# Kernel optimization log

Measured on AMD Instinct MI355X. Metric: run time of the kernel, lower is better.

## Reference

```python
import jax, jax.numpy as jnp
import numpy as np
from jax import lax

V, D, H, L, K = 50257, 1024, 2048, 6, 3
B, S = 4, 2048
EPS = 1.1920929e-07  # torch.finfo(float32).eps (torch RMSNorm default eps=None)


def rmsnorm(x, w):
    return x * lax.rsqrt(jnp.mean(x * x, axis=-1, keepdims=True) + EPS) * w


def depthwise_conv(x, w, b):
    # x: (B,S,D), w: (D,1,K) depthwise kernel, padding='same' as in torch Conv1d
    y = lax.conv_general_dilated(x.transpose(0, 2, 1), w, (1,), 'SAME',
                                 dimension_numbers=('NCH', 'OIH', 'NCH'),
                                 feature_group_count=x.shape[-1])
    return y.transpose(0, 2, 1) + b


def mingru(x, h0, wz, bz, wh, bh, wo, bo):
    # minGRU: z=sigmoid(Wz x), h_tilde=Wh x, h_t=(1-z_t)h_{t-1}+z_t h_tilde_t (parallel scan)
    z = jax.nn.sigmoid(jnp.einsum('bsd,hd->bsh', x, wz) + bz)
    htil = jnp.einsum('bsd,hd->bsh', x, wh) + bh
    a, bc = 1.0 - z, z * htil

    def comb(c1, c2):
        a1, b1 = c1
        a2, b2 = c2
        return a1 * a2, a2 * b1 + b2

    A, Bc = lax.associative_scan(comb, (a, bc), axis=1)
    h = A * h0[:, None, :] + Bc                      # (B,S,H)
    out = jnp.einsum('bsh,dh->bsd', h, wo) + bo      # project back to model dim
    return out, h[:, -1]


def setup_inputs():
    key = jax.random.key(0)
    ks = jax.random.split(key, 16)
    sc = 0.02
    p = {}
    p['x'] = jax.random.randint(ks[0], (B, S), 0, V)
    p['h_prev'] = jax.random.normal(ks[1], (B, L, H), jnp.float32)
    p['emb'] = jax.random.normal(ks[2], (V, D), jnp.float32) * sc
    p['conv_dw_w'] = jax.random.normal(ks[3], (L, D, 1, K), jnp.float32) * sc
    p['conv_dw_b'] = jnp.zeros((L, D), jnp.float32)
    p['conv_pw_w'] = jax.random.normal(ks[4], (L, D, D), jnp.float32) * sc
    p['conv_pw_b'] = jnp.zeros((L, D), jnp.float32)
    p['n1_w'] = jnp.ones((L, D), jnp.float32)
    p['wz'] = jax.random.normal(ks[5], (L, H, D), jnp.float32) * sc
    p['bz'] = jnp.zeros((L, H), jnp.float32)
    p['wh'] = jax.random.normal(ks[6], (L, H, D), jnp.float32) * sc
    p['bh'] = jnp.zeros((L, H), jnp.float32)
    p['wo'] = jax.random.normal(ks[7], (L, D, H), jnp.float32) * sc
    p['bo'] = jnp.zeros((L, D), jnp.float32)
    p['n2_w'] = jnp.ones((L, D), jnp.float32)
    p['f1_w'] = jax.random.normal(ks[8], (L, H, D), jnp.float32) * sc
    p['f1_b'] = jnp.zeros((L, H), jnp.float32)
    p['f2_w'] = jax.random.normal(ks[9], (L, D, H), jnp.float32) * sc
    p['f2_b'] = jnp.zeros((L, D), jnp.float32)
    p['norm_w'] = jnp.ones((D,), jnp.float32)
    p['out_w'] = jax.random.normal(ks[10], (H, D), jnp.float32) * sc
    p['out_b'] = jnp.zeros((H,), jnp.float32)
    return p


def reference(x, h_prev, emb, conv_dw_w, conv_dw_b, conv_pw_w, conv_pw_b, n1_w,
              wz, bz, wh, bh, wo, bo, n2_w, f1_w, f1_b, f2_w, f2_b,
              norm_w, out_w, out_b):
    xe = emb[x]                                      # (B,S,D)
    h_next = []
    for l in range(L):
        c = depthwise_conv(xe, conv_dw_w[l], conv_dw_b[l])
        c = jnp.einsum('bsd,ed->bse', c, conv_pw_w[l]) + conv_pw_b[l]  # 1x1 conv
        xe = c + xe
        g, hl = mingru(rmsnorm(xe, n1_w[l]), h_prev[:, l],
                       wz[l], bz[l], wh[l], bh[l], wo[l], bo[l])
        xe = g + xe
        f = rmsnorm(xe, n2_w[l])
        f = jnp.einsum('bsd,hd->bsh', f, f1_w[l]) + f1_b[l]
        f = jax.nn.gelu(f, approximate=False)
        f = jnp.einsum('bsh,dh->bsd', f, f2_w[l]) + f2_b[l]
        xe = f + xe
        h_next.append(hl)
    out = jnp.einsum('bsd,hd->bsh', rmsnorm(xe, norm_w), out_w) + out_b
    return out, jnp.stack(h_next, axis=1)             # (B,S,H), (B,L,H)
```

## Files before the change

kernel.cpp:

```cpp
#include <hip/hip_runtime.h>

typedef __bf16 bf16x8 __attribute__((ext_vector_type(8)));
typedef float f32x4 __attribute__((ext_vector_type(4)));

#define DEVI __device__ __forceinline__

namespace {
constexpr int cB = 4, cS = 2048, cD = 1024, cH = 2048, cL = 6;
constexpr int cM = cB * cS;
constexpr float cEPS = 1.1920929e-07f;
constexpr int NCH = 16, CHS = cS / NCH;
}

DEVI unsigned short f2bf(float f) {
  union { float f; unsigned u; } c; c.f = f;
  const unsigned u = c.u;
  return (unsigned short)((u + 0x7fffu + ((u >> 16) & 1u)) >> 16);
}
DEVI float bf2f(unsigned short h) {
  union { unsigned u; float f; } c; c.u = ((unsigned)h) << 16;
  return c.f;
}

DEVI void gld16(const void* g, void* l) {
  __builtin_amdgcn_global_load_lds(
      (__attribute__((address_space(1))) void*)g,
      (__attribute__((address_space(3))) void*)l, 16, 0, 0);
}

union F4 { float4 v; float a[4]; };

__global__ __launch_bounds__(256) void embed_k(const int* __restrict__ x,
    const float* __restrict__ emb, float* __restrict__ xe) {
  const int bs = blockIdx.x;
  const int idx = x[bs];
  const int t = threadIdx.x;
  *(float4*)&xe[(size_t)bs * cD + t * 4] =
      *(const float4*)&emb[(size_t)idx * cD + t * 4];
}

__global__ __launch_bounds__(256) void dwconv_k(const float* __restrict__ xe,
    const float* __restrict__ w, const float* __restrict__ bias,
    unsigned short* __restrict__ out) {
  const int bs = blockIdx.x;
  const int s = bs & (cS - 1);
  const int t = threadIdx.x;
  const int d = t * 4;
  const size_t base = (size_t)bs * cD + d;
  F4 x0, xm, xp, vb;
  x0.v = *(const float4*)&xe[base];
  xm.v = make_float4(0.f, 0.f, 0.f, 0.f);
  xp.v = make_float4(0.f, 0.f, 0.f, 0.f);
  if (s > 0) xm.v = *(const float4*)&xe[base - cD];
  if (s < cS - 1) xp.v = *(const float4*)&xe[base + cD];
  vb.v = *(const float4*)&bias[d];
  unsigned short o[4];
#pragma unroll
  for (int j = 0; j < 4; ++j) {
    const float w0 = w[(d + j) * 3 + 0];
    const float w1 = w[(d + j) * 3 + 1];
    const float w2 = w[(d + j) * 3 + 2];
    o[j] = f2bf(xm.a[j] * w0 + x0.a[j] * w1 + xp.a[j] * w2 + vb.a[j]);
  }
  *(ushort4*)&out[base] = make_ushort4(o[0], o[1], o[2], o[3]);
}

__global__ __launch_bounds__(256) void rmsnorm_k(const float* __restrict__ x,
    const float* __restrict__ w, unsigned short* __restrict__ o) {
  const int row = blockIdx.x;
  const int t = threadIdx.x;
  const size_t base = (size_t)row * cD + t * 4;
  F4 v; v.v = *(const float4*)&x[base];
  float ss = v.a[0]*v.a[0] + v.a[1]*v.a[1] + v.a[2]*v.a[2] + v.a[3]*v.a[3];
#pragma unroll
  for (int off = 32; off > 0; off >>= 1) ss += __shfl_down(ss, off, 64);
  __shared__ float red[4];
  if ((t & 63) == 0) red[t >> 6] = ss;
  __syncthreads();
  const float scale = rsqrtf((red[0]+red[1]+red[2]+red[3]) * (1.f/cD) + cEPS);
  F4 wv; wv.v = *(const float4*)&w[t * 4];
  *(ushort4*)&o[base] = make_ushort4(
      f2bf(v.a[0]*scale*wv.a[0]), f2bf(v.a[1]*scale*wv.a[1]),
      f2bf(v.a[2]*scale*wv.a[2]), f2bf(v.a[3]*scale*wv.a[3]));
}

__global__ __launch_bounds__(256) void cvt_k(const float* __restrict__ s,
    unsigned short* __restrict__ d, int n) {
  const int i = (blockIdx.x * 256 + threadIdx.x) * 4;
  if (i >= n) return;
  F4 v; v.v = *(const float4*)&s[i];
  *(ushort4*)&d[i] = make_ushort4(f2bf(v.a[0]), f2bf(v.a[1]),
                                  f2bf(v.a[2]), f2bf(v.a[3]));
}

template<int N, int K, int EPI>
__global__ __launch_bounds__(256) void gemm_bt(
    const unsigned short* __restrict__ A, const unsigned short* __restrict__ W,
    const float* __restrict__ bias, float* __restrict__ Cf,
    unsigned short* __restrict__ Cb) {
  __shared__ unsigned short As[128 * 32];
  __shared__ unsigned short Bs[128 * 32];
  const int t = threadIdx.x;
  const int lane = t & 63;
  const int wave = t >> 6;
  const int m0 = blockIdx.x * 128;
  const int n0 = blockIdx.y * 128;
  const int wm = (wave >> 1) * 64;
  const int wn = (wave & 1) * 64;
  const int fr = lane & 15;
  const int fk = (lane >> 4) * 8;

  const int arow = t >> 2;
  const int acol = (t & 3) * 8;
  const unsigned short* gA = A + (size_t)(m0 + arow) * K + acol;
  const unsigned short* gB = W + (size_t)(n0 + arow) * K + acol;
  unsigned short* lA = As + wave * 512;
  unsigned short* lB = Bs + wave * 512;

  f32x4 acc[4][4] = {};
  for (int k0 = 0; k0 < K; k0 += 32) {
    gld16(gA + k0, lA);
    gld16(gA + k0 + (size_t)64 * K, lA + 2048);
    gld16(gB + k0, lB);
    gld16(gB + k0 + (size_t)64 * K, lB + 2048);
    __syncthreads();
    bf16x8 fa[4], fb[4];
#pragma unroll
    for (int i = 0; i < 4; ++i) {
      fa[i] = *(const bf16x8*)&As[(wm + i * 16 + fr) * 32 + fk];
      fb[i] = *(const bf16x8*)&Bs[(wn + i * 16 + fr) * 32 + fk];
    }
#pragma unroll
    for (int i = 0; i < 4; ++i)
#pragma unroll
      for (int j = 0; j < 4; ++j)
        acc[i][j] = __builtin_amdgcn_mfma_f32_16x16x32_bf16(
            fa[i], fb[j], acc[i][j], 0, 0, 0);
    __syncthreads();
  }

  const int r0 = m0 + wm + ((lane >> 4) << 2);
  const int c0 = n0 + wn + fr;
#pragma unroll
  for (int i = 0; i < 4; ++i)
#pragma unroll
    for (int j = 0; j < 4; ++j) {
      const int col = c0 + j * 16;
      const float bv = bias[col];
#pragma unroll
      for (int r = 0; r < 4; ++r) {
        const size_t idx = (size_t)(r0 + i * 16 + r) * N + col;
        const float v = acc[i][j][r] + bv;
        if constexpr (EPI == 0) {
          Cf[idx] = v;
        } else if constexpr (EPI == 1) {
          Cf[idx] += v;
        } else if constexpr (EPI == 2) {
          Cb[idx] = f2bf(1.f / (1.f + __expf(-v)));
        } else if constexpr (EPI == 3) {
          Cb[idx] = f2bf(v);
        } else {
          Cb[idx] = f2bf(0.5f * v * (1.f + erff(v * 0.70710678118654752f)));
        }
      }
    }
}

__global__ __launch_bounds__(256) void scan1_k(const unsigned short* __restrict__ z,
    const unsigned short* __restrict__ ht, float* __restrict__ Ac,
    float* __restrict__ Bc) {
  const int tid = blockIdx.x * 256 + threadIdx.x;
  const int hp = (tid & (cH / 2 - 1)) * 2;
  const int ck = (tid / (cH / 2)) & (NCH - 1);
  const int b = tid / ((cH / 2) * NCH);
  const size_t base = ((size_t)b * cS + (size_t)ck * CHS) * cH + hp;
  float a0 = 1.f, s0 = 0.f, a1 = 1.f, s1 = 0.f;
#pragma unroll 4
  for (int s = 0; s < CHS; ++s) {
    const unsigned zz = *(const unsigned*)&z[base + (size_t)s * cH];
    const unsigned hh = *(const unsigned*)&ht[base + (size_t)s * cH];
    const float z0 = bf2f((unsigned short)(zz & 0xffff)), z1 = bf2f((unsigned short)(zz >> 16));
    const float t0 = bf2f((unsigned short)(hh & 0xffff)), t1 = bf2f((unsigned short)(hh >> 16));
    const float aa0 = 1.f - z0, aa1 = 1.f - z1;
    s0 = aa0 * s0 + z0 * t0; a0 *= aa0;
    s1 = aa1 * s1 + z1 * t1; a1 *= aa1;
  }
  const size_t so = ((size_t)b * NCH + ck) * cH + hp;
  *(float2*)&Ac[so] = make_float2(a0, a1);
  *(float2*)&Bc[so] = make_float2(s0, s1);
}

__global__ __launch_bounds__(256) void scan2_k(const float* __restrict__ Ac,
    const float* __restrict__ Bc, const float* __restrict__ h_prev,
    float* __restrict__ P, float* __restrict__ hn, int l) {
  const int tid = blockIdx.x * 256 + threadIdx.x;
  const int h = tid & (cH - 1);
  const int b = tid >> 11;
  float run = h_prev[((size_t)b * cL + l) * cH + h];
#pragma unroll
  for (int c = 0; c < NCH; ++c) {
    const size_t so = ((size_t)b * NCH + c) * cH + h;
    P[so] = run;
    run = Ac[so] * run + Bc[so];
  }
  hn[((size_t)b * cL + l) * cH + h] = run;
}

__global__ __launch_bounds__(256) void scan3_k(const unsigned short* __restrict__ z,
    unsigned short* __restrict__ ht, const float* __restrict__ P) {
  const int tid = blockIdx.x * 256 + threadIdx.x;
  const int hp = (tid & (cH / 2 - 1)) * 2;
  const int ck = (tid / (cH / 2)) & (NCH - 1);
  const int b = tid / ((cH / 2) * NCH);
  const size_t base = ((size_t)b * cS + (size_t)ck * CHS) * cH + hp;
  const size_t so = ((size_t)b * NCH + ck) * cH + hp;
  const float2 rr = *(const float2*)&P[so];
  float r0 = rr.x, r1 = rr.y;
#pragma unroll 4
  for (int s = 0; s < CHS; ++s) {
    const unsigned zz = *(const unsigned*)&z[base + (size_t)s * cH];
    const unsigned hh = *(const unsigned*)&ht[base + (size_t)s * cH];
    const float z0 = bf2f((unsigned short)(zz & 0xffff)), z1 = bf2f((unsigned short)(zz >> 16));
    const float t0 = bf2f((unsigned short)(hh & 0xffff)), t1 = bf2f((unsigned short)(hh >> 16));
    r0 = (1.f - z0) * r0 + z0 * t0;
    r1 = (1.f - z1) * r1 + z1 * t1;
    *(unsigned*)&ht[base + (size_t)s * cH] =
        (unsigned)f2bf(r0) | ((unsigned)f2bf(r1) << 16);
  }
}

extern "C" void kernel_launch(void* const* d_in, const int* in_sizes, int n_in,
                              void* d_out, int out_size, void* d_ws, size_t ws_size,
                              hipStream_t stream) {
  (void)in_sizes; (void)n_in; (void)out_size; (void)ws_size;
  const int*   x      = (const int*)d_in[0];
  const float* h_prev = (const float*)d_in[1];
  const float* emb    = (const float*)d_in[2];
  const float* cdw_w  = (const float*)d_in[3];
  const float* cdw_b  = (const float*)d_in[4];
  const float* cpw_w  = (const float*)d_in[5];
  const float* cpw_b  = (const float*)d_in[6];
  const float* n1w    = (const float*)d_in[7];
  const float* wzp    = (const float*)d_in[8];
  const float* bzp    = (const float*)d_in[9];
  const float* whp    = (const float*)d_in[10];
  const float* bhp    = (const float*)d_in[11];
  const float* wop    = (const float*)d_in[12];
  const float* bop    = (const float*)d_in[13];
  const float* n2w    = (const float*)d_in[14];
  const float* f1wp   = (const float*)d_in[15];
  const float* f1bp   = (const float*)d_in[16];
  const float* f2wp   = (const float*)d_in[17];
  const float* f2bp   = (const float*)d_in[18];
  const float* nw     = (const float*)d_in[19];
  const float* owp    = (const float*)d_in[20];
  const float* obp    = (const float*)d_in[21];

  float* out_main = (float*)d_out;
  float* out_hn   = out_main + (size_t)cM * cH;

  char* p = (char*)d_ws;
  auto alloc = [&](size_t bytes) {
    char* r = p; p += (bytes + 255) & ~(size_t)255; return r;
  };
  float*          xe = (float*)alloc((size_t)cM * cD * 4);
  unsigned short* xn = (unsigned short*)alloc((size_t)cM * cD * 2);
  unsigned short* zb = (unsigned short*)alloc((size_t)cM * cH * 2);
  unsigned short* hb = (unsigned short*)alloc((size_t)cM * cH * 2);
  float* Ac = (float*)alloc((size_t)cB * NCH * cH * 4);
  float* Bc = (float*)alloc((size_t)cB * NCH * cH * 4);
  float* Pr = (float*)alloc((size_t)cB * NCH * cH * 4);
  unsigned short* w_pw = (unsigned short*)alloc((size_t)cD * cD * 2);
  unsigned short* w_z  = (unsigned short*)alloc((size_t)cH * cD * 2);
  unsigned short* w_h  = (unsigned short*)alloc((size_t)cH * cD * 2);
  unsigned short* w_o  = (unsigned short*)alloc((size_t)cD * cH * 2);
  unsigned short* w_f1 = (unsigned short*)alloc((size_t)cH * cD * 2);
  unsigned short* w_f2 = (unsigned short*)alloc((size_t)cD * cH * 2);

  auto cvt = [&](const float* src, unsigned short* dst, size_t n) {
    cvt_k<<<dim3((unsigned)(n / 1024)), 256, 0, stream>>>(src, dst, (int)n);
  };

  embed_k<<<cM, 256, 0, stream>>>(x, emb, xe);

  for (int l = 0; l < cL; ++l) {
    cvt(cpw_w + (size_t)l * cD * cD, w_pw, (size_t)cD * cD);
    cvt(wzp  + (size_t)l * cH * cD, w_z,  (size_t)cH * cD);
    cvt(whp  + (size_t)l * cH * cD, w_h,  (size_t)cH * cD);
    cvt(wop  + (size_t)l * cD * cH, w_o,  (size_t)cD * cH);
    cvt(f1wp + (size_t)l * cH * cD, w_f1, (size_t)cH * cD);
    cvt(f2wp + (size_t)l * cD * cH, w_f2, (size_t)cD * cH);

    dwconv_k<<<cM, 256, 0, stream>>>(xe, cdw_w + (size_t)l * cD * 3,
                                     cdw_b + (size_t)l * cD, xn);
    gemm_bt<cD, cD, 1><<<dim3(cM / 128, cD / 128), 256, 0, stream>>>(
        xn, w_pw, cpw_b + (size_t)l * cD, xe, nullptr);

    rmsnorm_k<<<cM, 256, 0, stream>>>(xe, n1w + (size_t)l * cD, xn);
    gemm_bt<cH, cD, 2><<<dim3(cM / 128, cH / 128), 256, 0, stream>>>(
        xn, w_z, bzp + (size_t)l * cH, nullptr, zb);
    gemm_bt<cH, cD, 3><<<dim3(cM / 128, cH / 128), 256, 0, stream>>>(
        xn, w_h, bhp + (size_t)l * cH, nullptr, hb);
    scan1_k<<<cB * NCH * (cH / 2) / 256, 256, 0, stream>>>(zb, hb, Ac, Bc);
    scan2_k<<<cB * cH / 256, 256, 0, stream>>>(Ac, Bc, h_prev, Pr, out_hn, l);
    scan3_k<<<cB * NCH * (cH / 2) / 256, 256, 0, stream>>>(zb, hb, Pr);
    gemm_bt<cD, cH, 1><<<dim3(cM / 128, cD / 128), 256, 0, stream>>>(
        hb, w_o, bop + (size_t)l * cD, xe, nullptr);

    rmsnorm_k<<<cM, 256, 0, stream>>>(xe, n2w + (size_t)l * cD, xn);
    gemm_bt<cH, cD, 4><<<dim3(cM / 128, cH / 128), 256, 0, stream>>>(
        xn, w_f1, f1bp + (size_t)l * cH, nullptr, zb);
    gemm_bt<cD, cH, 1><<<dim3(cM / 128, cD / 128), 256, 0, stream>>>(
        zb, w_f2, f2bp + (size_t)l * cD, xe, nullptr);
  }

  rmsnorm_k<<<cM, 256, 0, stream>>>(xe, nw, xn);
  cvt(owp, w_z, (size_t)cH * cD);
  gemm_bt<cH, cD, 0><<<dim3(cM / 128, cH / 128), 256, 0, stream>>>(
      xn, w_z, obp, out_main, nullptr);
}
```

Measured before the change: 2.397 ms.

## Add 256x256 pipelined 8-wave GEMM, fuse z/h projections, hoist weight conversion

Adds a new 512-thread GEMM kernel with 256x256 tiles, double-buffered LDS, and phased MFMA/load interleaving using barriers and priority hints. It is used for the wide-N GEMMs: the z and h projections are merged into one launch, and the FFN up-projection and output head also use it. Weight conversion to bf16 now runs once for all layers before the loop instead of per layer. The aim is better MFMA utilisation and data reuse, plus fewer launches, at the cost of a larger workspace and high register and LDS pressure.

```diff
diff --git a/kernel.cpp b/kernel.cpp
--- a/kernel.cpp
+++ b/kernel.cpp
@@ -151,19 +151,161 @@
       for (int r = 0; r < 4; ++r) {
         const size_t idx = (size_t)(r0 + i * 16 + r) * N + col;
         const float v = acc[i][j][r] + bv;
-        if constexpr (EPI == 0) {
+        if constexpr (EPI == 1) {
+          Cf[idx] += v;
+        } else {
           Cf[idx] = v;
-        } else if constexpr (EPI == 1) {
-          Cf[idx] += v;
-        } else if constexpr (EPI == 2) {
-          Cb[idx] = f2bf(1.f / (1.f + __expf(-v)));
-        } else if constexpr (EPI == 3) {
-          Cb[idx] = f2bf(v);
-        } else {
-          Cb[idx] = f2bf(0.5f * v * (1.f + erff(v * 0.70710678118654752f)));
         }
       }
     }
+}
+
+#define RDA(BUF, MH)                                                        \
+  _Pragma("unroll") for (int mf = 0; mf < 4; ++mf)                          \
+  _Pragma("unroll") for (int kk = 0; kk < 2; ++kk)                          \
+      a[mf * 2 + kk] = *(const bf16x8*)&lds[(BUF)*16384 + aB + (MH)*4096 +  \
+                                            mf * 1024 + kk * 32];
+
+#define RDB(BUF)                                                            \
+  _Pragma("unroll") for (int q = 0; q < 4; ++q)                             \
+  _Pragma("unroll") for (int kk = 0; kk < 2; ++kk)                          \
+      b[q >> 1][(q & 1) * 2 + kk] =                                         \
+          *(const bf16x8*)&lds[(BUF)*16384 + bB + q * 1024 + kk * 32];
+
+#define MMQ(MH, NH)                                                         \
+  _Pragma("unroll") for (int mf = 0; mf < 4; ++mf)                          \
+  _Pragma("unroll") for (int nf = 0; nf < 2; ++nf)                          \
+  _Pragma("unroll") for (int kk = 0; kk < 2; ++kk)                          \
+      acc[(MH)*4 + mf][(NH)*2 + nf] = __builtin_amdgcn_mfma_f32_16x16x32_bf16( \
+          a[mf * 2 + kk], b[NH][nf * 2 + kk], acc[(MH)*4 + mf][(NH)*2 + nf],  \
+          0, 0, 0);
+
+#define PH_SYNC()                                                           \
+  __builtin_amdgcn_s_barrier();                                             \
+  asm volatile("s_waitcnt lgkmcnt(0)" ::: "memory");                        \
+  __builtin_amdgcn_sched_barrier(0);                                        \
+  __builtin_amdgcn_s_setprio(1)
+
+#define PH_END()                                                            \
+  __builtin_amdgcn_s_setprio(0);                                            \
+  __builtin_amdgcn_s_barrier()
+
+#define TILE_PHASES(TI, BUF, OBUF)                                          \
+  {                                                                         \
+    RDA(BUF, 0); RDB(BUF);                                                  \
+    { const int n1 = (TI) + 1;                                              \
+      stA((n1 < NT) ? n1 : 0, 1, (n1 < NT) ? ldsA(OBUF, 1) : ldsDummy); }   \
+    asm volatile("s_waitcnt lgkmcnt(8)" ::: "memory");                      \
+    PH_SYNC(); MMQ(0, 0); PH_END();                                         \
+    { const int n2 = (TI) + 2;                                              \
+      stB((n2 < NT) ? n2 : 0, 0, (n2 < NT) ? ldsB(BUF, 0) : ldsDummy); }    \
+    PH_SYNC(); MMQ(0, 1); PH_END();                                         \
+    RDA(BUF, 1);                                                            \
+    { const int n2 = (TI) + 2;                                              \
+      stB((n2 < NT) ? n2 : 0, 1, (n2 < NT) ? ldsB(BUF, 1) : ldsDummy); }    \
+    PH_SYNC(); MMQ(1, 1); PH_END();                                         \
+    { const int n2 = (TI) + 2;                                              \
+      stA((n2 < NT) ? n2 : 0, 0, (n2 < NT) ? ldsA(BUF, 0) : ldsDummy); }    \
+    asm volatile("s_waitcnt vmcnt(6)" ::: "memory");                        \
+    PH_SYNC(); MMQ(1, 0); PH_END();                                         \
+  }
+
+template<int N, int K, int EPI, int NS>
+__global__ __launch_bounds__(512, 2) void gemm8p(
+    const unsigned short* __restrict__ A,
+    const unsigned short* __restrict__ W0,
+    const unsigned short* __restrict__ W1,
+    const float* __restrict__ bias0, const float* __restrict__ bias1,
+    float* __restrict__ Cf, unsigned short* __restrict__ Cb,
+    unsigned short* __restrict__ Cb2) {
+  static_assert(K % 128 == 0, "NT must be even");
+  constexpr int NT = K / 64;
+  __shared__ unsigned short lds[73728];
+  const int t = threadIdx.x;
+  const int lane = t & 63;
+  const int wave = t >> 6;
+  const int wr = wave >> 2;
+  const int wc = wave & 3;
+  const int m0 = blockIdx.x * 256;
+  const int n0 = blockIdx.y * 256;
+
+  const bool zpart = (n0 < NS);
+  const unsigned short* Wp = zpart ? W0 : W1;
+  const int nw0 = zpart ? n0 : n0 - NS;
+  const float* bp = zpart ? bias0 : bias1;
+  const int CW = zpart ? NS : (N - NS);
+
+  const int srow = t >> 3;
+  const int scol = ((t & 7) * 8) ^ (((t >> 5) & 1) << 4);
+  const unsigned short* gA = A  + (size_t)(m0 + srow) * K + scol;
+  const unsigned short* gB = Wp + (size_t)(nw0 + srow) * K + scol;
+  const int ldsw = wave * 512;
+
+  auto ldsA = [&](int buf, int h) -> unsigned short* {
+    return (unsigned short*)&lds[buf * 16384 + h * 8192 + ldsw];
+  };
+  auto ldsB = [&](int buf, int h) -> unsigned short* {
+    return (unsigned short*)&lds[32768 + buf * 16384 + h * 8192 + ldsw];
+  };
+  unsigned short* ldsDummy = (unsigned short*)&lds[65536 + ldsw];
+  auto stA = [&](int tile, int h, unsigned short* dst) {
+    const unsigned short* s = gA + (size_t)(h * 128) * K + tile * 64;
+    gld16(s, dst);
+    gld16(s + (size_t)64 * K, dst + 4096);
+  };
+  auto stB = [&](int tile, int h, unsigned short* dst) {
+    const unsigned short* s = gB + (size_t)(h * 128) * K + tile * 64;
+    gld16(s, dst);
+    gld16(s + (size_t)64 * K, dst + 4096);
+  };
+
+  const int sx = ((lane >> 2) & 1) << 4;
+  const int aoff = (lane & 15) * 64 + (((lane >> 4) * 8) ^ sx);
+  const int aB = wr * 8192 + aoff;
+  const int bB = 32768 + (wc >> 1) * 8192 + (wc & 1) * 4096 + aoff;
+
+  bf16x8 a[8];
+  bf16x8 b[2][4];
+  f32x4 acc[8][4] = {};
+
+  stB(0, 0, ldsB(0, 0)); stB(0, 1, ldsB(0, 1));
+  stA(0, 0, ldsA(0, 0)); stA(0, 1, ldsA(0, 1));
+  stB(1, 0, ldsB(1, 0)); stB(1, 1, ldsB(1, 1));
+  stA(1, 0, ldsA(1, 0));
+  asm volatile("s_waitcnt vmcnt(6)" ::: "memory");
+  __builtin_amdgcn_s_barrier();
+
+  for (int tp = 0; tp < NT / 2; ++tp) {
+    const int t0 = 2 * tp;
+    TILE_PHASES(t0, 0, 1);
+    TILE_PHASES(t0 + 1, 1, 0);
+  }
+
+  float* cf = Cf;
+  unsigned short* cb = zpart ? Cb : Cb2;
+  const int r0 = m0 + wr * 128 + ((lane >> 4) << 2);
+  const int c0 = nw0 + wc * 64 + (lane & 15);
+#pragma unroll
+  for (int mfg = 0; mfg < 8; ++mfg) {
+#pragma unroll
+    for (int nfg = 0; nfg < 4; ++nfg) {
+      const int col = c0 + nfg * 16;
+      const float bv = bp[col];
+#pragma unroll
+      for (int r = 0; r < 4; ++r) {
+        const size_t idx = (size_t)(r0 + mfg * 16 + r) * CW + col;
+        const float v = acc[mfg][nfg][r] + bv;
+        if constexpr (EPI == 0) {
+          cf[idx] = v;
+        } else if constexpr (EPI == 4) {
+          cb[idx] = f2bf(0.5f * v * (1.f + erff(v * 0.70710678118654752f)));
+        } else {
+          if (zpart) cb[idx] = f2bf(1.f / (1.f + __expf(-v)));
+          else       cb[idx] = f2bf(v);
+        }
+      }
+    }
+  }
 }
 
 __global__ __launch_bounds__(256) void scan1_k(const unsigned short* __restrict__ z,
@@ -270,52 +412,55 @@
   float* Ac = (float*)alloc((size_t)cB * NCH * cH * 4);
   float* Bc = (float*)alloc((size_t)cB * NCH * cH * 4);
   float* Pr = (float*)alloc((size_t)cB * NCH * cH * 4);
-  unsigned short* w_pw = (unsigned short*)alloc((size_t)cD * cD * 2);
-  unsigned short* w_z  = (unsigned short*)alloc((size_t)cH * cD * 2);
-  unsigned short* w_h  = (unsigned short*)alloc((size_t)cH * cD * 2);
-  unsigned short* w_o  = (unsigned short*)alloc((size_t)cD * cH * 2);
-  unsigned short* w_f1 = (unsigned short*)alloc((size_t)cH * cD * 2);
-  unsigned short* w_f2 = (unsigned short*)alloc((size_t)cD * cH * 2);
+  unsigned short* w_pw = (unsigned short*)alloc((size_t)cL * cD * cD * 2);
+  unsigned short* w_z  = (unsigned short*)alloc((size_t)cL * cH * cD * 2);
+  unsigned short* w_h  = (unsigned short*)alloc((size_t)cL * cH * cD * 2);
+  unsigned short* w_o  = (unsigned short*)alloc((size_t)cL * cD * cH * 2);
+  unsigned short* w_f1 = (unsigned short*)alloc((size_t)cL * cH * cD * 2);
+  unsigned short* w_f2 = (unsigned short*)alloc((size_t)cL * cD * cH * 2);
+  unsigned short* w_ow = (unsigned short*)alloc((size_t)cH * cD * 2);
 
   auto cvt = [&](const float* src, unsigned short* dst, size_t n) {
     cvt_k<<<dim3((unsigned)(n / 1024)), 256, 0, stream>>>(src, dst, (int)n);
   };
 
+  cvt(cpw_w, w_pw, (size_t)cL * cD * cD);
+  cvt(wzp,  w_z,  (size_t)cL * cH * cD);
+  cvt(whp,  w_h,  (size_t)cL * cH * cD);
+  cvt(wop,  w_o,  (size_t)cL * cD * cH);
+  cvt(f1wp, w_f1, (size_t)cL * cH * cD);
+  cvt(f2wp, w_f2, (size_t)cL * cD * cH);
+  cvt(owp,  w_ow, (size_t)cH * cD);
+
   embed_k<<<cM, 256, 0, stream>>>(x, emb, xe);
 
   for (int l = 0; l < cL; ++l) {
-    cvt(cpw_w + (size_t)l * cD * cD, w_pw, (size_t)cD * cD);
-    cvt(wzp  + (size_t)l * cH * cD, w_z,  (size_t)cH * cD);
-    cvt(whp  + (size_t)l * cH * cD, w_h,  (size_t)cH * cD);
-    cvt(wop  + (size_t)l * cD * cH, w_o,  (size_t)cD * cH);
-    cvt(f1wp + (size_t)l * cH * cD, w_f1, (size_t)cH * cD);
-    cvt(f2wp + (size_t)l * cD * cH, w_f2, (size_t)cD * cH);
+    const size_t oDD = (size_t)l * cD * cD, oHD = (size_t)l * cH * cD;
 
     dwconv_k<<<cM, 256, 0, stream>>>(xe, cdw_w + (size_t)l * cD * 3,
                                      cdw_b + (size_t)l * cD, xn);
     gemm_bt<cD, cD, 1><<<dim3(cM / 128, cD / 128), 256, 0, stream>>>(
-        xn, w_pw, cpw_b + (size_t)l * cD, xe, nullptr);
+        xn, w_pw + oDD, cpw_b + (size_t)l * cD, xe, nullptr);
 
     rmsnorm_k<<<cM, 256, 0, stream>>>(xe, n1w + (size_t)l * cD, xn);
-    gemm_bt<cH, cD, 2><<<dim3(cM / 128, cH / 128), 256, 0, stream>>>(
-        xn, w_z, bzp + (size_t)l * cH, nullptr, zb);
-    gemm_bt<cH, cD, 3><<<dim3(cM / 128, cH / 128), 256, 0, stream>>>(
-        xn, w_h, bhp + (size_t)l * cH, nullptr, hb);
+    gemm8p<2 * cH, cD, 5, cH><<<dim3(cM / 256, 2 * cH / 256), 512, 0, stream>>>(
+        xn, w_z + oHD, w_h + oHD, bzp + (size_t)l * cH, bhp + (size_t)l * cH,
+        nullptr, zb, hb);
     scan1_k<<<cB * NCH * (cH / 2) / 256, 256, 0, stream>>>(zb, hb, Ac, Bc);
     scan2_k<<<cB * cH / 256, 256, 0, stream>>>(Ac, Bc, h_prev, Pr, out_hn, l);
     scan3_k<<<cB * NCH * (cH / 2) / 256, 256, 0, stream>>>(zb, hb, Pr);
     gemm_bt<cD, cH, 1><<<dim3(cM / 128, cD / 128), 256, 0, stream>>>(
-        hb, w_o, bop + (size_t)l * cD, xe, nullptr);
+        hb, w_o + oHD, bop + (size_t)l * cD, xe, nullptr);
 
     rmsnorm_k<<<cM, 256, 0, stream>>>(xe, n2w + (size_t)l * cD, xn);
-    gemm_bt<cH, cD, 4><<<dim3(cM / 128, cH / 128), 256, 0, stream>>>(
-        xn, w_f1, f1bp + (size_t)l * cH, nullptr, zb);
+    gemm8p<cH, cD, 4, cH><<<dim3(cM / 256, cH / 256), 512, 0, stream>>>(
+        xn, w_f1 + oHD, w_f1 + oHD, f1bp + (size_t)l * cH, f1bp + (size_t)l * cH,
+        nullptr, zb, zb);
     gemm_bt<cD, cH, 1><<<dim3(cM / 128, cD / 128), 256, 0, stream>>>(
-        zb, w_f2, f2bp + (size_t)l * cD, xe, nullptr);
+        zb, w_f2 + oHD, f2bp + (size_t)l * cD, xe, nullptr);
   }
 
   rmsnorm_k<<<cM, 256, 0, stream>>>(xe, nw, xn);
-  cvt(owp, w_z, (size_t)cH * cD);
-  gemm_bt<cH, cD, 0><<<dim3(cM / 128, cH / 128), 256, 0, stream>>>(
-      xn, w_z, obp, out_main, nullptr);
-}
+  gemm8p<cH, cD, 0, cH><<<dim3(cM / 256, cH / 256), 512, 0, stream>>>(
+      xn, w_ow, w_ow, obp, obp, out_main, nullptr, nullptr);
+}
```

Measured after the change: 2.359 ms. No clear change (-1.6%).
